# Kernel optimization log

Measured on AMD Instinct MI355X. Metric: run time of the kernel, lower is better.

The kernel has to match this reference:

```python
import jax, jax.numpy as jnp
import numpy as np
import math

D_MODEL = 1024
N_HEADS = 16
D_K = D_MODEL // N_HEADS
MAX_REL = 128


def setup_inputs() -> dict:
    key = jax.random.key(0)
    ks = jax.random.split(key, 10)
    B, S = 2, 2048
    std = 1.0 / math.sqrt(D_MODEL)
    inp = {
        "x": jax.random.normal(ks[0], (B, S, D_MODEL), dtype=jnp.float32),
        "Wq": jax.random.normal(ks[1], (D_MODEL, D_MODEL), dtype=jnp.float32) * std,
        "bq": jnp.zeros((D_MODEL,), dtype=jnp.float32),
        "Wk": jax.random.normal(ks[2], (D_MODEL, D_MODEL), dtype=jnp.float32) * std,
        "bk": jnp.zeros((D_MODEL,), dtype=jnp.float32),
        "Wv": jax.random.normal(ks[3], (D_MODEL, D_MODEL), dtype=jnp.float32) * std,
        "bv": jnp.zeros((D_MODEL,), dtype=jnp.float32),
        "Wo": jax.random.normal(ks[4], (D_MODEL, D_MODEL), dtype=jnp.float32) * std,
        "bo": jnp.zeros((D_MODEL,), dtype=jnp.float32),
        "rel_bias": jax.random.normal(ks[5], (N_HEADS, 2 * MAX_REL + 1), dtype=jnp.float32) * 0.02,
    }
    return inp


def _rel_bias_matrix(rel_bias, seq_len):
    # (H, S, S) gathered relative-position bias
    pos = jnp.arange(seq_len)
    rel = pos[:, None] - pos[None, :]
    idx = jnp.clip(rel, -MAX_REL, MAX_REL) + MAX_REL  # (S, S) in [0, 2M]
    return rel_bias[:, idx]  # (H, S, S)


def reference(x, Wq, bq, Wk, bk, Wv, bv, Wo, bo, rel_bias):
    B, S, _ = x.shape
    def proj(W, b):
        y = x @ W.T + b  # torch Linear: x @ W^T + b
        return y.reshape(B, S, N_HEADS, D_K).transpose(0, 2, 1, 3)  # (B,H,S,Dk)
    Q, K, V = proj(Wq, bq), proj(Wk, bk), proj(Wv, bv)
    scores = jnp.einsum("bhqd,bhkd->bhqk", Q, K) / math.sqrt(D_K)
    scores = scores + _rel_bias_matrix(rel_bias, S)[None]
    attn = jax.nn.softmax(scores, axis=-1)
    out = jnp.einsum("bhqk,bhkd->bhqd", attn, V)
    out = out.transpose(0, 2, 1, 3).reshape(B, S, D_MODEL)
    return out @ Wo.T + bo
```

## Files before the change

### kernel.cpp

```cpp
#include <hip/hip_runtime.h>

static constexpr int DM = 1024;
static constexpr int NH = 16;
static constexpr int DK = 64;
static constexpr int S  = 2048;
static constexpr int B  = 2;
static constexpr float LOG2E = 1.4426950408889634f;
static constexpr float FMAX  = 11.0f;

typedef _Float16 f16;
typedef _Float16 f16x8 __attribute__((ext_vector_type(8)));
typedef _Float16 f16x4 __attribute__((ext_vector_type(4)));
typedef float    f32x4 __attribute__((ext_vector_type(4)));

static constexpr size_t NX = (size_t)B * S * DM;
static constexpr size_t NW = (size_t)DM * DM;

__global__ __launch_bounds__(256) void cvt_f16(const float* __restrict__ x,
                                               const float* __restrict__ wq,
                                               const float* __restrict__ wk,
                                               const float* __restrict__ wv,
                                               const float* __restrict__ wo,
                                               f16* __restrict__ xh,
                                               f16* __restrict__ wqh,
                                               f16* __restrict__ wkh,
                                               f16* __restrict__ wvh,
                                               f16* __restrict__ woh)
{
    const size_t base = ((size_t)blockIdx.x * 256 + threadIdx.x) * 8;
    const float* src; f16* dst; size_t off;
    if (base < NX) { src = x; dst = xh; off = base; }
    else {
        const size_t rem = base - NX;
        const int seg = (int)(rem >> 20);
        off = rem & (NW - 1);
        src = seg == 0 ? wq : (seg == 1 ? wk : (seg == 2 ? wv : wo));
        dst = seg == 0 ? wqh : (seg == 1 ? wkh : (seg == 2 ? wvh : woh));
    }
    float4 a = *(const float4*)&src[off];
    float4 b = *(const float4*)&src[off + 4];
    f16x8 h = { (f16)a.x, (f16)a.y, (f16)a.z, (f16)a.w,
                (f16)b.x, (f16)b.y, (f16)b.z, (f16)b.w };
    *(f16x8*)&dst[off] = h;
}

template<int MODE>
__global__ __launch_bounds__(256) void gemm_h(const f16* __restrict__ A,
                                              const f16* __restrict__ W0,
                                              const f16* __restrict__ W1,
                                              const f16* __restrict__ W2,
                                              const float* __restrict__ b0,
                                              const float* __restrict__ b1,
                                              const float* __restrict__ b2,
                                              void* __restrict__ o0,
                                              void* __restrict__ o1,
                                              void* __restrict__ o2)
{
    __shared__ f16 As[128 * 72];
    __shared__ f16 Bs[128 * 72];

    const int t    = threadIdx.x;
    const int w    = t >> 6;
    const int lane = t & 63;
    const int tx   = lane & 15;
    const int quad = lane >> 4;
    const int wm   = w >> 1;
    const int wn   = w & 1;
    const int m0   = blockIdx.y * 128;

    const f16* W; const float* bias; f16* outh = nullptr; float* outf = nullptr;
    float scale; int n0;
    if (MODE == 0) {
        const int wsel = blockIdx.x >> 3;
        n0   = (blockIdx.x & 7) * 128;
        W    = wsel == 0 ? W0 : (wsel == 1 ? W1 : W2);
        bias = wsel == 0 ? b0 : (wsel == 1 ? b1 : b2);
        outh = (f16*)(wsel == 0 ? o0 : (wsel == 1 ? o1 : o2));
        scale = wsel == 0 ? LOG2E * 0.125f : 1.0f;
    } else {
        n0 = blockIdx.x * 128;
        W = W0; bias = b0; outf = (float*)o0; scale = 1.0f;
    }

    const int lr = t >> 2;
    const int lc = (t & 3) * 8;

    f32x4 acc[4][4];
#pragma unroll
    for (int mt = 0; mt < 4; ++mt)
#pragma unroll
        for (int nt = 0; nt < 4; ++nt) acc[mt][nt] = (f32x4){0.f, 0.f, 0.f, 0.f};

    f16x8 ga[4], gb[4];
    {
        const f16* Ap = A + (size_t)(m0 + lr) * DM + lc;
        const f16* Wp = W + (size_t)(n0 + lr) * DM + lc;
        ga[0] = *(const f16x8*)(Ap);
        ga[1] = *(const f16x8*)(Ap + 32);
        ga[2] = *(const f16x8*)(Ap + (size_t)64 * DM);
        ga[3] = *(const f16x8*)(Ap + (size_t)64 * DM + 32);
        gb[0] = *(const f16x8*)(Wp);
        gb[1] = *(const f16x8*)(Wp + 32);
        gb[2] = *(const f16x8*)(Wp + (size_t)64 * DM);
        gb[3] = *(const f16x8*)(Wp + (size_t)64 * DM + 32);
    }

    for (int k0 = 0; k0 < DM; k0 += 64) {
        __syncthreads();
        *(f16x8*)&As[ lr       * 72 + lc     ] = ga[0];
        *(f16x8*)&As[ lr       * 72 + lc + 32] = ga[1];
        *(f16x8*)&As[(lr + 64) * 72 + lc     ] = ga[2];
        *(f16x8*)&As[(lr + 64) * 72 + lc + 32] = ga[3];
        *(f16x8*)&Bs[ lr       * 72 + lc     ] = gb[0];
        *(f16x8*)&Bs[ lr       * 72 + lc + 32] = gb[1];
        *(f16x8*)&Bs[(lr + 64) * 72 + lc     ] = gb[2];
        *(f16x8*)&Bs[(lr + 64) * 72 + lc + 32] = gb[3];
        if (k0 + 64 < DM) {
            const f16* Ap = A + (size_t)(m0 + lr) * DM + k0 + 64 + lc;
            const f16* Wp = W + (size_t)(n0 + lr) * DM + k0 + 64 + lc;
            ga[0] = *(const f16x8*)(Ap);
            ga[1] = *(const f16x8*)(Ap + 32);
            ga[2] = *(const f16x8*)(Ap + (size_t)64 * DM);
            ga[3] = *(const f16x8*)(Ap + (size_t)64 * DM + 32);
            gb[0] = *(const f16x8*)(Wp);
            gb[1] = *(const f16x8*)(Wp + 32);
            gb[2] = *(const f16x8*)(Wp + (size_t)64 * DM);
            gb[3] = *(const f16x8*)(Wp + (size_t)64 * DM + 32);
        }
        __syncthreads();

        f16x8 af[4][2];
#pragma unroll
        for (int mt = 0; mt < 4; ++mt)
#pragma unroll
            for (int ks = 0; ks < 2; ++ks)
                af[mt][ks] = *(const f16x8*)&As[(wm*64 + mt*16 + tx)*72 + ks*32 + quad*8];
#pragma unroll
        for (int nt = 0; nt < 4; ++nt) {
#pragma unroll
            for (int ks = 0; ks < 2; ++ks) {
                f16x8 bf = *(const f16x8*)&Bs[(wn*64 + nt*16 + tx)*72 + ks*32 + quad*8];
#pragma unroll
                for (int mt = 0; mt < 4; ++mt)
                    acc[mt][nt] = __builtin_amdgcn_mfma_f32_16x16x32_f16(af[mt][ks], bf, acc[mt][nt], 0, 0, 0);
            }
        }
    }

#pragma unroll
    for (int nt = 0; nt < 4; ++nt) {
        const int n = n0 + wn*64 + nt*16 + tx;
        const float bn = bias[n];
#pragma unroll
        for (int mt = 0; mt < 4; ++mt)
#pragma unroll
            for (int r = 0; r < 4; ++r) {
                const int m = m0 + wm*64 + mt*16 + quad*4 + r;
                const float v = (acc[mt][nt][r] + bn) * scale;
                if (MODE == 0) {
                    const int bi = m >> 11;
                    const int ss = m & (S - 1);
                    const int h  = n >> 6;
                    const int dk = n & (DK - 1);
                    outh[((size_t)((bi*NH + h)*S + ss))*DK + dk] = (f16)v;
                } else {
                    outf[(size_t)m * DM + n] = v;
                }
            }
    }
}

__global__ __launch_bounds__(256, 4) void attn_v3(const f16* __restrict__ Q,
                                                  const f16* __restrict__ K,
                                                  const f16* __restrict__ V,
                                                  const float* __restrict__ relb,
                                                  float* __restrict__ On,
                                                  float* __restrict__ lp)
{
    __shared__ f16 Ks[64*72];
    __shared__ f16 Vt[64*72];
    __shared__ float rb2[257];

    const int t    = threadIdx.x;
    const int w    = t >> 6;
    const int lane = t & 63;
    const int tx   = lane & 15;
    const int quad = lane >> 4;
    const int qt   = blockIdx.x >> 1;
    const int sp   = blockIdx.x & 1;
    const int h    = blockIdx.y;
    const int b    = blockIdx.z;
    const int q0   = qt * 128;

    const f16* Qb = Q + (size_t)((b*NH + h) * S) * DK;
    const f16* Kb = K + (size_t)((b*NH + h) * S) * DK;
    const f16* Vb = V + (size_t)((b*NH + h) * S) * DK;

    for (int i = t; i < 257; i += 256) rb2[i] = relb[h*257 + i] * LOG2E - FMAX;

    const int qrow = q0 + w*32 + tx;
    f16x8 qf[2][2];
#pragma unroll
    for (int qb = 0; qb < 2; ++qb)
#pragma unroll
        for (int ks = 0; ks < 2; ++ks)
            qf[qb][ks] = *(const f16x8*)(Qb + (size_t)(qrow + qb*16)*DK + ks*32 + quad*8);

    f32x4 oT[4][2];
    float lsum[2] = {0.f, 0.f};
#pragma unroll
    for (int d = 0; d < 4; ++d)
#pragma unroll
        for (int qb = 0; qb < 2; ++qb) oT[d][qb] = (f32x4){0.f, 0.f, 0.f, 0.f};

    const int kt0 = sp * (S/128);
    for (int kt = kt0; kt < kt0 + S/128; ++kt) {
        const int k0 = kt * 64;

        const int seq = t & 63, d0k = (t >> 6) * 16;
        f16x8 kr0 = *(const f16x8*)(Kb + (size_t)(k0 + seq)*DK + d0k);
        f16x8 kr1 = *(const f16x8*)(Kb + (size_t)(k0 + seq)*DK + d0k + 8);
        const int s2 = (t & 31) * 2, d0v = (t >> 5) * 8;
        f16x8 vr0 = *(const f16x8*)(Vb + (size_t)(k0 + s2    )*DK + d0v);
        f16x8 vr1 = *(const f16x8*)(Vb + (size_t)(k0 + s2 + 1)*DK + d0v);

        __syncthreads();
        *(f16x8*)&Ks[seq*72 + d0k    ] = kr0;
        *(f16x8*)&Ks[seq*72 + d0k + 8] = kr1;
        {
            const int g = ((s2 >> 2) & 3)*16 + (s2 >> 4)*4 + (s2 & 3);
            const unsigned short* u0 = (const unsigned short*)&vr0;
            const unsigned short* u1 = (const unsigned short*)&vr1;
#pragma unroll
            for (int j = 0; j < 8; ++j) {
                unsigned int pw = (unsigned int)u0[j] | ((unsigned int)u1[j] << 16);
                *(unsigned int*)&Vt[(d0v + j)*72 + g] = pw;
            }
        }
        __syncthreads();

        const bool farlo = (k0 - q0) >= 256;
        const bool farhi = (q0 - k0) >= 192;
        const float bconst = farlo ? rb2[0] : rb2[256];
        const int relbase = (q0 + w*32 + tx) - (k0 + quad*4);

        f16x4 pf[4][2];
#pragma unroll
        for (int sb = 0; sb < 4; ++sb) {
            f32x4 sT[2] = {(f32x4){0.f,0.f,0.f,0.f}, (f32x4){0.f,0.f,0.f,0.f}};
#pragma unroll
            for (int ks = 0; ks < 2; ++ks) {
                f16x8 kf = *(const f16x8*)&Ks[(sb*16 + tx)*72 + ks*32 + quad*8];
#pragma unroll
                for (int qb = 0; qb < 2; ++qb)
                    sT[qb] = __builtin_amdgcn_mfma_f32_16x16x32_f16(kf, qf[qb][ks], sT[qb], 0, 0, 0);
            }
            if (farlo | farhi) {
#pragma unroll
                for (int qb = 0; qb < 2; ++qb)
#pragma unroll
                    for (int r = 0; r < 4; ++r) {
                        const float p = exp2f(sT[qb][r] + bconst);
                        lsum[qb] += p;
                        pf[sb][qb][r] = (f16)p;
                    }
            } else {
#pragma unroll
                for (int qb = 0; qb < 2; ++qb)
#pragma unroll
                    for (int r = 0; r < 4; ++r) {
                        int rel = relbase + qb*16 - sb*16 - r;
                        rel = rel < -128 ? -128 : (rel > 128 ? 128 : rel);
                        const float p = exp2f(sT[qb][r] + rb2[rel + 128]);
                        lsum[qb] += p;
                        pf[sb][qb][r] = (f16)p;
                    }
            }
        }

#pragma unroll
        for (int d = 0; d < 4; ++d) {
#pragma unroll
            for (int sp2 = 0; sp2 < 2; ++sp2) {
                f16x8 vv = *(const f16x8*)&Vt[(d*16 + tx)*72 + quad*16 + sp2*8];
                f16x4 vlo = __builtin_shufflevector(vv, vv, 0, 1, 2, 3);
                f16x4 vhi = __builtin_shufflevector(vv, vv, 4, 5, 6, 7);
#pragma unroll
                for (int qb = 0; qb < 2; ++qb) {
                    oT[d][qb] = __builtin_amdgcn_mfma_f32_16x16x16f16(vlo, pf[sp2*2    ][qb], oT[d][qb], 0, 0, 0);
                    oT[d][qb] = __builtin_amdgcn_mfma_f32_16x16x16f16(vhi, pf[sp2*2 + 1][qb], oT[d][qb], 0, 0, 0);
                }
            }
        }
    }

#pragma unroll
    for (int qb = 0; qb < 2; ++qb) {
        float l = lsum[qb];
        l += __shfl_xor(l, 16);
        l += __shfl_xor(l, 32);
        const int q = q0 + w*32 + qb*16 + tx;
        if (quad == 0)
            lp[(((size_t)sp*B + b)*NH + h)*S + q] = l;
#pragma unroll
        for (int d = 0; d < 4; ++d)
            *(f32x4*)&On[(size_t)sp*NX + ((size_t)(b*S + q))*DM + h*DK + d*16 + quad*4] = oT[d][qb];
    }
}

__global__ __launch_bounds__(256) void combine(const float* __restrict__ On,
                                               const float* __restrict__ lp,
                                               f16* __restrict__ AOh)
{
    const size_t i8 = ((size_t)blockIdx.x * 256 + threadIdx.x) * 8;
    const int token = (int)(i8 >> 10);
    const int c     = (int)(i8 & (DM - 1));
    const int b     = token >> 11;
    const int st    = token & (S - 1);
    const int h     = c >> 6;
    const float l = lp[((size_t)b*NH + h)*S + st]
                  + lp[(((size_t)B + b)*NH + h)*S + st];
    const float inv = 1.0f / l;
    float4 a0 = *(const float4*)&On[i8];
    float4 a1 = *(const float4*)&On[i8 + 4];
    float4 b0 = *(const float4*)&On[NX + i8];
    float4 b1 = *(const float4*)&On[NX + i8 + 4];
    f16x8 o = { (f16)((a0.x + b0.x) * inv), (f16)((a0.y + b0.y) * inv),
                (f16)((a0.z + b0.z) * inv), (f16)((a0.w + b0.w) * inv),
                (f16)((a1.x + b1.x) * inv), (f16)((a1.y + b1.y) * inv),
                (f16)((a1.z + b1.z) * inv), (f16)((a1.w + b1.w) * inv) };
    *(f16x8*)&AOh[i8] = o;
}

extern "C" void kernel_launch(void* const* d_in, const int* in_sizes, int n_in,
                              void* d_out, int out_size, void* d_ws, size_t ws_size,
                              hipStream_t stream)
{
    const float* x    = (const float*)d_in[0];
    const float* Wq   = (const float*)d_in[1];
    const float* bq   = (const float*)d_in[2];
    const float* Wk   = (const float*)d_in[3];
    const float* bk   = (const float*)d_in[4];
    const float* Wv   = (const float*)d_in[5];
    const float* bv   = (const float*)d_in[6];
    const float* Wo   = (const float*)d_in[7];
    const float* bo   = (const float*)d_in[8];
    const float* relb = (const float*)d_in[9];

    f16* Xh  = (f16*)d_ws;
    f16* Wqh = Xh  + NX;
    f16* Wkh = Wqh + NW;
    f16* Wvh = Wkh + NW;
    f16* Woh = Wvh + NW;
    f16* Qh  = Woh + NW;
    f16* Kh  = Qh  + NX;
    f16* Vh  = Kh  + NX;
    f16* AOh = Vh  + NX;
    float* On = (float*)(AOh + NX);
    float* lpart = On + 2*NX;

    cvt_f16<<<(NX + 4*NW) / (256*8), 256, 0, stream>>>(x, Wq, Wk, Wv, Wo,
                                                       Xh, Wqh, Wkh, Wvh, Woh);
    gemm_h<0><<<dim3(24, 32), 256, 0, stream>>>(Xh, Wqh, Wkh, Wvh,
                                                bq, bk, bv, Qh, Kh, Vh);
    attn_v3<<<dim3((S/128)*2, NH, B), 256, 0, stream>>>(Qh, Kh, Vh, relb, On, lpart);
    combine<<<NX / (256*8), 256, 0, stream>>>(On, lpart, AOh);
    gemm_h<1><<<dim3(8, 32), 256, 0, stream>>>(AOh, Woh, nullptr, nullptr,
                                               bo, nullptr, nullptr,
                                               d_out, nullptr, nullptr);
}
```

Before: 220.0 us.

## Load GEMM tiles directly into LDS with XOR-swizzled layout

Replaces the register-staged global loads (prefetched one iteration ahead) in the projection GEMMs with global_load_lds direct-to-LDS transfers. The padded 72-wide LDS rows become unpadded 64-wide rows with an XOR chunk swizzle to avoid bank conflicts, and launch bounds request 4 blocks per CU. This cuts VGPR pressure and LDS footprint to raise occupancy, but it drops the software prefetch overlap, so each iteration now waits on its own global loads.

```diff
diff --git a/kernel.cpp b/kernel.cpp
--- a/kernel.cpp
+++ b/kernel.cpp
@@ -15,6 +15,13 @@
 
 static constexpr size_t NX = (size_t)B * S * DM;
 static constexpr size_t NW = (size_t)DM * DM;
+
+__device__ __forceinline__ void gload16(f16* lds, const f16* g) {
+    __builtin_amdgcn_global_load_lds(
+        (__attribute__((address_space(1))) void*)g,
+        (__attribute__((address_space(3))) void*)lds,
+        16, 0, 0);
+}
 
 __global__ __launch_bounds__(256) void cvt_f16(const float* __restrict__ x,
                                                const float* __restrict__ wq,
@@ -45,19 +52,19 @@
 }
 
 template<int MODE>
-__global__ __launch_bounds__(256) void gemm_h(const f16* __restrict__ A,
-                                              const f16* __restrict__ W0,
-                                              const f16* __restrict__ W1,
-                                              const f16* __restrict__ W2,
-                                              const float* __restrict__ b0,
-                                              const float* __restrict__ b1,
-                                              const float* __restrict__ b2,
-                                              void* __restrict__ o0,
-                                              void* __restrict__ o1,
-                                              void* __restrict__ o2)
-{
-    __shared__ f16 As[128 * 72];
-    __shared__ f16 Bs[128 * 72];
+__global__ __launch_bounds__(256, 4) void gemm_h(const f16* __restrict__ A,
+                                                 const f16* __restrict__ W0,
+                                                 const f16* __restrict__ W1,
+                                                 const f16* __restrict__ W2,
+                                                 const float* __restrict__ b0,
+                                                 const float* __restrict__ b1,
+                                                 const float* __restrict__ b2,
+                                                 void* __restrict__ o0,
+                                                 void* __restrict__ o1,
+                                                 void* __restrict__ o2)
+{
+    __shared__ f16 As[128 * 64];
+    __shared__ f16 Bs[128 * 64];
 
     const int t    = threadIdx.x;
     const int w    = t >> 6;
@@ -82,50 +89,25 @@
         W = W0; bias = b0; outf = (float*)o0; scale = 1.0f;
     }
 
-    const int lr = t >> 2;
-    const int lc = (t & 3) * 8;
+    const int lrow = lane >> 3;
+    const int lchk = (lane & 7) ^ lrow;
+    const f16* Ag = A + (size_t)(m0 + w*32 + lrow) * DM + lchk * 8;
+    const f16* Bg = W + (size_t)(n0 + w*32 + lrow) * DM + lchk * 8;
+    f16* Abase = &As[(w*32) * 64];
+    f16* Bbase = &Bs[(w*32) * 64];
 
     f32x4 acc[4][4];
 #pragma unroll
     for (int mt = 0; mt < 4; ++mt)
 #pragma unroll
         for (int nt = 0; nt < 4; ++nt) acc[mt][nt] = (f32x4){0.f, 0.f, 0.f, 0.f};
-
-    f16x8 ga[4], gb[4];
-    {
-        const f16* Ap = A + (size_t)(m0 + lr) * DM + lc;
-        const f16* Wp = W + (size_t)(n0 + lr) * DM + lc;
-        ga[0] = *(const f16x8*)(Ap);
-        ga[1] = *(const f16x8*)(Ap + 32);
-        ga[2] = *(const f16x8*)(Ap + (size_t)64 * DM);
-        ga[3] = *(const f16x8*)(Ap + (size_t)64 * DM + 32);
-        gb[0] = *(const f16x8*)(Wp);
-        gb[1] = *(const f16x8*)(Wp + 32);
-        gb[2] = *(const f16x8*)(Wp + (size_t)64 * DM);
-        gb[3] = *(const f16x8*)(Wp + (size_t)64 * DM + 32);
-    }
 
     for (int k0 = 0; k0 < DM; k0 += 64) {
         __syncthreads();
-        *(f16x8*)&As[ lr       * 72 + lc     ] = ga[0];
-        *(f16x8*)&As[ lr       * 72 + lc + 32] = ga[1];
-        *(f16x8*)&As[(lr + 64) * 72 + lc     ] = ga[2];
-        *(f16x8*)&As[(lr + 64) * 72 + lc + 32] = ga[3];
-        *(f16x8*)&Bs[ lr       * 72 + lc     ] = gb[0];
-        *(f16x8*)&Bs[ lr       * 72 + lc + 32] = gb[1];
-        *(f16x8*)&Bs[(lr + 64) * 72 + lc     ] = gb[2];
-        *(f16x8*)&Bs[(lr + 64) * 72 + lc + 32] = gb[3];
-        if (k0 + 64 < DM) {
-            const f16* Ap = A + (size_t)(m0 + lr) * DM + k0 + 64 + lc;
-            const f16* Wp = W + (size_t)(n0 + lr) * DM + k0 + 64 + lc;
-            ga[0] = *(const f16x8*)(Ap);
-            ga[1] = *(const f16x8*)(Ap + 32);
-            ga[2] = *(const f16x8*)(Ap + (size_t)64 * DM);
-            ga[3] = *(const f16x8*)(Ap + (size_t)64 * DM + 32);
-            gb[0] = *(const f16x8*)(Wp);
-            gb[1] = *(const f16x8*)(Wp + 32);
-            gb[2] = *(const f16x8*)(Wp + (size_t)64 * DM);
-            gb[3] = *(const f16x8*)(Wp + (size_t)64 * DM + 32);
+#pragma unroll
+        for (int i = 0; i < 4; ++i) {
+            gload16(Abase + i*512, Ag + k0 + (size_t)(i*8) * DM);
+            gload16(Bbase + i*512, Bg + k0 + (size_t)(i*8) * DM);
         }
         __syncthreads();
 
@@ -134,12 +116,14 @@
         for (int mt = 0; mt < 4; ++mt)
 #pragma unroll
             for (int ks = 0; ks < 2; ++ks)
-                af[mt][ks] = *(const f16x8*)&As[(wm*64 + mt*16 + tx)*72 + ks*32 + quad*8];
+                af[mt][ks] = *(const f16x8*)&As[(wm*64 + mt*16 + tx)*64
+                                               + (((ks*4 + quad) ^ (tx & 7)) * 8)];
 #pragma unroll
         for (int nt = 0; nt < 4; ++nt) {
 #pragma unroll
             for (int ks = 0; ks < 2; ++ks) {
-                f16x8 bf = *(const f16x8*)&Bs[(wn*64 + nt*16 + tx)*72 + ks*32 + quad*8];
+                f16x8 bf = *(const f16x8*)&Bs[(wn*64 + nt*16 + tx)*64
+                                              + (((ks*4 + quad) ^ (tx & 7)) * 8)];
 #pragma unroll
                 for (int mt = 0; mt < 4; ++mt)
                     acc[mt][nt] = __builtin_amdgcn_mfma_f32_16x16x32_f16(af[mt][ks], bf, acc[mt][nt], 0, 0, 0);
```

Result: slower. 227.4 us (+3.4%).

## Split attention keys four ways, store fp16 partials, fold bias into MFMA accumulator

Applied to the files above, without the earlier changes.

Raises the key-sequence split in the attention kernel from two to four, so four times as many blocks cover the sequence for more parallelism on the GPU. Partial outputs are now stored in fp16 instead of fp32, which keeps the combine traffic roughly level despite the extra splits. The relative-position bias is preloaded into the MFMA accumulator, which removes a separate add after the matmul. Risks include a larger combine kernel and added fp16 rounding of unnormalised partial sums.

```diff
diff --git a/kernel.cpp b/kernel.cpp
--- a/kernel.cpp
+++ b/kernel.cpp
@@ -7,6 +7,7 @@
 static constexpr int B  = 2;
 static constexpr float LOG2E = 1.4426950408889634f;
 static constexpr float FMAX  = 11.0f;
+static constexpr int NSPLIT = 4;
 
 typedef _Float16 f16;
 typedef _Float16 f16x8 __attribute__((ext_vector_type(8)));
@@ -170,11 +171,11 @@
     }
 }
 
-__global__ __launch_bounds__(256, 4) void attn_v3(const f16* __restrict__ Q,
+__global__ __launch_bounds__(256, 4) void attn_v4(const f16* __restrict__ Q,
                                                   const f16* __restrict__ K,
                                                   const f16* __restrict__ V,
                                                   const float* __restrict__ relb,
-                                                  float* __restrict__ On,
+                                                  f16* __restrict__ On,
                                                   float* __restrict__ lp)
 {
     __shared__ f16 Ks[64*72];
@@ -186,8 +187,8 @@
     const int lane = t & 63;
     const int tx   = lane & 15;
     const int quad = lane >> 4;
-    const int qt   = blockIdx.x >> 1;
-    const int sp   = blockIdx.x & 1;
+    const int qt   = blockIdx.x >> 2;
+    const int sp   = blockIdx.x & 3;
     const int h    = blockIdx.y;
     const int b    = blockIdx.z;
     const int q0   = qt * 128;
@@ -213,8 +214,8 @@
 #pragma unroll
         for (int qb = 0; qb < 2; ++qb) oT[d][qb] = (f32x4){0.f, 0.f, 0.f, 0.f};
 
-    const int kt0 = sp * (S/128);
-    for (int kt = kt0; kt < kt0 + S/128; ++kt) {
+    const int kt0 = sp * (S / 64 / NSPLIT);
+    for (int kt = kt0; kt < kt0 + S/64/NSPLIT; ++kt) {
         const int k0 = kt * 64;
 
         const int seq = t & 63, d0k = (t >> 6) * 16;
@@ -247,23 +248,10 @@
         f16x4 pf[4][2];
 #pragma unroll
         for (int sb = 0; sb < 4; ++sb) {
-            f32x4 sT[2] = {(f32x4){0.f,0.f,0.f,0.f}, (f32x4){0.f,0.f,0.f,0.f}};
-#pragma unroll
-            for (int ks = 0; ks < 2; ++ks) {
-                f16x8 kf = *(const f16x8*)&Ks[(sb*16 + tx)*72 + ks*32 + quad*8];
-#pragma unroll
-                for (int qb = 0; qb < 2; ++qb)
-                    sT[qb] = __builtin_amdgcn_mfma_f32_16x16x32_f16(kf, qf[qb][ks], sT[qb], 0, 0, 0);
-            }
+            f32x4 sT[2];
             if (farlo | farhi) {
-#pragma unroll
-                for (int qb = 0; qb < 2; ++qb)
-#pragma unroll
-                    for (int r = 0; r < 4; ++r) {
-                        const float p = exp2f(sT[qb][r] + bconst);
-                        lsum[qb] += p;
-                        pf[sb][qb][r] = (f16)p;
-                    }
+                sT[0] = (f32x4){bconst, bconst, bconst, bconst};
+                sT[1] = sT[0];
             } else {
 #pragma unroll
                 for (int qb = 0; qb < 2; ++qb)
@@ -271,11 +259,24 @@
                     for (int r = 0; r < 4; ++r) {
                         int rel = relbase + qb*16 - sb*16 - r;
                         rel = rel < -128 ? -128 : (rel > 128 ? 128 : rel);
-                        const float p = exp2f(sT[qb][r] + rb2[rel + 128]);
-                        lsum[qb] += p;
-                        pf[sb][qb][r] = (f16)p;
+                        sT[qb][r] = rb2[rel + 128];
                     }
             }
+#pragma unroll
+            for (int ks = 0; ks < 2; ++ks) {
+                f16x8 kf = *(const f16x8*)&Ks[(sb*16 + tx)*72 + ks*32 + quad*8];
+#pragma unroll
+                for (int qb = 0; qb < 2; ++qb)
+                    sT[qb] = __builtin_amdgcn_mfma_f32_16x16x32_f16(kf, qf[qb][ks], sT[qb], 0, 0, 0);
+            }
+#pragma unroll
+            for (int qb = 0; qb < 2; ++qb)
+#pragma unroll
+                for (int r = 0; r < 4; ++r) {
+                    const float p = exp2f(sT[qb][r]);
+                    lsum[qb] += p;
+                    pf[sb][qb][r] = (f16)p;
+                }
         }
 
 #pragma unroll
@@ -303,12 +304,15 @@
         if (quad == 0)
             lp[(((size_t)sp*B + b)*NH + h)*S + q] = l;
 #pragma unroll
-        for (int d = 0; d < 4; ++d)
-            *(f32x4*)&On[(size_t)sp*NX + ((size_t)(b*S + q))*DM + h*DK + d*16 + quad*4] = oT[d][qb];
-    }
-}
-
-__global__ __launch_bounds__(256) void combine(const float* __restrict__ On,
+        for (int d = 0; d < 4; ++d) {
+            f16x4 hv = { (f16)oT[d][qb][0], (f16)oT[d][qb][1],
+                         (f16)oT[d][qb][2], (f16)oT[d][qb][3] };
+            *(f16x4*)&On[(size_t)sp*NX + ((size_t)(b*S + q))*DM + h*DK + d*16 + quad*4] = hv;
+        }
+    }
+}
+
+__global__ __launch_bounds__(256) void combine(const f16* __restrict__ On,
                                                const float* __restrict__ lp,
                                                f16* __restrict__ AOh)
 {
@@ -318,17 +322,23 @@
     const int b     = token >> 11;
     const int st    = token & (S - 1);
     const int h     = c >> 6;
-    const float l = lp[((size_t)b*NH + h)*S + st]
-                  + lp[(((size_t)B + b)*NH + h)*S + st];
+    float l = 0.f;
+#pragma unroll
+    for (int sp = 0; sp < NSPLIT; ++sp)
+        l += lp[(((size_t)sp*B + b)*NH + h)*S + st];
     const float inv = 1.0f / l;
-    float4 a0 = *(const float4*)&On[i8];
-    float4 a1 = *(const float4*)&On[i8 + 4];
-    float4 b0 = *(const float4*)&On[NX + i8];
-    float4 b1 = *(const float4*)&On[NX + i8 + 4];
-    f16x8 o = { (f16)((a0.x + b0.x) * inv), (f16)((a0.y + b0.y) * inv),
-                (f16)((a0.z + b0.z) * inv), (f16)((a0.w + b0.w) * inv),
-                (f16)((a1.x + b1.x) * inv), (f16)((a1.y + b1.y) * inv),
-                (f16)((a1.z + b1.z) * inv), (f16)((a1.w + b1.w) * inv) };
+    float acc[8];
+#pragma unroll
+    for (int j = 0; j < 8; ++j) acc[j] = 0.f;
+#pragma unroll
+    for (int sp = 0; sp < NSPLIT; ++sp) {
+        f16x8 v = *(const f16x8*)&On[(size_t)sp*NX + i8];
+#pragma unroll
+        for (int j = 0; j < 8; ++j) acc[j] += (float)v[j];
+    }
+    f16x8 o;
+#pragma unroll
+    for (int j = 0; j < 8; ++j) o[j] = (f16)(acc[j] * inv);
     *(f16x8*)&AOh[i8] = o;
 }
 
@@ -356,14 +366,14 @@
     f16* Kh  = Qh  + NX;
     f16* Vh  = Kh  + NX;
     f16* AOh = Vh  + NX;
-    float* On = (float*)(AOh + NX);
-    float* lpart = On + 2*NX;
+    f16* On  = AOh + NX;
+    float* lpart = (float*)(On + (size_t)NSPLIT*NX);
 
     cvt_f16<<<(NX + 4*NW) / (256*8), 256, 0, stream>>>(x, Wq, Wk, Wv, Wo,
                                                        Xh, Wqh, Wkh, Wvh, Woh);
     gemm_h<0><<<dim3(24, 32), 256, 0, stream>>>(Xh, Wqh, Wkh, Wvh,
                                                 bq, bk, bv, Qh, Kh, Vh);
-    attn_v3<<<dim3((S/128)*2, NH, B), 256, 0, stream>>>(Qh, Kh, Vh, relb, On, lpart);
+    attn_v4<<<dim3((S/128)*NSPLIT, NH, B), 256, 0, stream>>>(Qh, Kh, Vh, relb, On, lpart);
     combine<<<NX / (256*8), 256, 0, stream>>>(On, lpart, AOh);
     gemm_h<1><<<dim3(8, 32), 256, 0, stream>>>(AOh, Woh, nullptr, nullptr,
                                                bo, nullptr, nullptr,
```

Result: no change. 221.2 us (+0.5%).
